# Performance work log

Hardware: AMD Instinct MI355X
Metric: run time of the kernel (lower is better)

The kernel has to match this reference:

```python
import jax, jax.numpy as jnp
import numpy as np

C = 64  # in_channels == out_channels (required by final view)

def setup_inputs() -> dict:
    key = jax.random.key(0)
    ks = jax.random.split(key, 7)
    x = jax.random.normal(ks[0], (2, C, 16, 16, 16), dtype=jnp.float32)
    s = 1.0 / np.sqrt(C)
    Wq = jax.random.uniform(ks[1], (C, C), jnp.float32, -s, s)
    bq = jax.random.uniform(ks[2], (C,), jnp.float32, -s, s)
    Wk = jax.random.uniform(ks[3], (C, C), jnp.float32, -s, s)
    bk = jax.random.uniform(ks[4], (C,), jnp.float32, -s, s)
    Wv = jax.random.uniform(ks[5], (C, C), jnp.float32, -s, s)
    bv = jax.random.uniform(ks[6], (C,), jnp.float32, -s, s)
    return {"x": x, "Wq": Wq, "bq": bq, "Wk": Wk, "bk": bk, "Wv": Wv, "bv": bv}

def _proj(x, W, b):
    # 1x1x1 Conv3d == per-voxel channel GEMM; x: [B,C,D,H,W]
    return jnp.einsum('oc,bcdhw->bodhw', W, x) + b[None, :, None, None, None]

def reference(x, Wq, bq, Wk, bk, Wv, bv):
    B, Cin, D, H, W = x.shape
    q = _proj(x, Wq, bq).reshape(B, C, -1)  # [B,C,N]
    k = _proj(x, Wk, bk).reshape(B, C, -1)
    v = _proj(x, Wv, bv).reshape(B, C, -1)
    # attention[b,i,j] = softmax_j(q_i . k_j); NOTE: unscaled, as in the source
    attn = jax.nn.softmax(jnp.einsum('bci,bcj->bij', q, k), axis=-1)
    out = jnp.einsum('bcj,bij->bci', v, attn)  # out_i = sum_j a_ij v_j
    return out.reshape(x.shape)
```

## Files before the change

### kernel.cpp

```cpp
#include <hip/hip_runtime.h>
#include <math.h>

#define CCH 64
#define NVOX 4096
#define NB 2
#define RS 72
#define TS 136

typedef _Float16 f16x8 __attribute__((ext_vector_type(8)));
typedef _Float16 f16x4 __attribute__((ext_vector_type(4)));
typedef __fp16   g16x2 __attribute__((ext_vector_type(2)));
typedef float f32x4 __attribute__((ext_vector_type(4)));

__global__ __launch_bounds__(256) void qkv_proj(
    const float* __restrict__ x,
    const float* __restrict__ Wq, const float* __restrict__ bq,
    const float* __restrict__ Wk, const float* __restrict__ bk,
    const float* __restrict__ Wv, const float* __restrict__ bv,
    _Float16* __restrict__ qh, _Float16* __restrict__ kh, _Float16* __restrict__ vh)
{
    __shared__ float Ws[3 * 64 * 64];
    __shared__ float xs[64 * 32];
    const int t  = threadIdx.x;
    const int b  = blockIdx.x >> 7;
    const int i0 = (blockIdx.x & 127) * 32;

    {
        const float4* Wq4 = (const float4*)Wq;
        const float4* Wk4 = (const float4*)Wk;
        const float4* Wv4 = (const float4*)Wv;
        float4* Ws4 = (float4*)Ws;
#pragma unroll
        for (int s = 0; s < 4; ++s) {
            int idx = t + 256 * s;
            Ws4[idx]        = Wq4[idx];
            Ws4[1024 + idx] = Wk4[idx];
            Ws4[2048 + idx] = Wv4[idx];
        }
    }
    {
        int cc = t >> 2;
        int m0 = (t & 3) * 8;
        const float* src = x + ((b * CCH + cc) * NVOX) + i0 + m0;
#pragma unroll
        for (int s = 0; s < 8; ++s) xs[cc * 32 + m0 + s] = src[s];
    }
    __syncthreads();

    const int vox = t & 31;
    const int c0  = (t >> 5) * 8;

#pragma unroll
    for (int m = 0; m < 3; ++m) {
        const float* Wm  = &Ws[m * 4096];
        const float* bia = (m == 0) ? bq : (m == 1) ? bk : bv;
        float acc[8];
#pragma unroll
        for (int j = 0; j < 8; ++j) acc[j] = bia[c0 + j];
        for (int cc = 0; cc < 64; cc += 4) {
            float xv0 = xs[(cc + 0) * 32 + vox];
            float xv1 = xs[(cc + 1) * 32 + vox];
            float xv2 = xs[(cc + 2) * 32 + vox];
            float xv3 = xs[(cc + 3) * 32 + vox];
#pragma unroll
            for (int j = 0; j < 8; ++j) {
                float4 w = *(const float4*)&Wm[(c0 + j) * 64 + cc];
                acc[j] = fmaf(w.x, xv0, acc[j]);
                acc[j] = fmaf(w.y, xv1, acc[j]);
                acc[j] = fmaf(w.z, xv2, acc[j]);
                acc[j] = fmaf(w.w, xv3, acc[j]);
            }
        }
        if (m < 2) {
            f16x8 hv;
#pragma unroll
            for (int j = 0; j < 8; ++j) hv[j] = (_Float16)acc[j];
            _Float16* dst = ((m == 0) ? qh : kh) + ((b * NVOX) + i0 + vox) * CCH + c0;
            *(f16x8*)dst = hv;
        } else {
#pragma unroll
            for (int j = 0; j < 8; ++j)
                vh[(b * CCH + c0 + j) * NVOX + i0 + vox] = (_Float16)acc[j];
        }
    }
}

template <int SPLIT>
__global__ __launch_bounds__(256) void attn(
    const _Float16* __restrict__ qh, const _Float16* __restrict__ kh,
    const _Float16* __restrict__ vh,
    _Float16* __restrict__ po,
    float* __restrict__ ml,
    float* __restrict__ out)
{
    __shared__ _Float16 ksl[2][64 * RS];
    __shared__ _Float16 vsl[2][64 * RS];

    constexpr int LS = (SPLIT == 8) ? 3 : (SPLIT == 4) ? 2 : (SPLIT == 2) ? 1 : 0;
    const int t    = threadIdx.x;
    const int h    = blockIdx.x & (SPLIT - 1);
    const int tile = blockIdx.x >> LS;
    const int b    = tile >> 5;
    const int i0   = (tile & 31) * 128;

    const int lane = t & 63;
    const int w    = t >> 6;
    const int q4   = lane >> 4;
    const int n    = lane & 15;

    const int row = t >> 2;
    const int c0  = (t & 3) * 16;
    const int JT  = 64 / SPLIT;

    auto load_tile = [&](int jt, float4 r[4]) {
        const int j0 = (h * JT + jt) * 64;
        const float4* ks = (const float4*)&kh[((size_t)(b * NVOX) + j0 + row) * CCH + c0];
        r[0] = ks[0]; r[1] = ks[1];
        const float4* vs = (const float4*)&vh[((size_t)b * CCH + row) * NVOX + j0 + c0];
        r[2] = vs[0]; r[3] = vs[1];
    };
    auto store_tile = [&](int buf, const float4 r[4]) {
        *(float4*)&ksl[buf][row * RS + c0]     = r[0];
        *(float4*)&ksl[buf][row * RS + c0 + 8] = r[1];
        *(float4*)&vsl[buf][row * RS + c0]     = r[2];
        *(float4*)&vsl[buf][row * RS + c0 + 8] = r[3];
    };

    f16x8 aq[2][2];
#pragma unroll
    for (int g = 0; g < 2; ++g) {
        const _Float16* qrow =
            qh + ((size_t)(b * NVOX) + i0 + w * 32 + g * 16 + n) * CCH + q4 * 8;
        aq[g][0] = *(const f16x8*)(qrow);
        aq[g][1] = *(const f16x8*)(qrow + 32);
    }

    float4 stg[4];
    load_tile(0, stg);
    store_tile(0, stg);

    float m_prev[2] = {-1e30f, -1e30f}, l[2] = {0.f, 0.f};
    f32x4 o[2][4];
#pragma unroll
    for (int g = 0; g < 2; ++g)
#pragma unroll
        for (int mt = 0; mt < 4; ++mt) o[g][mt] = (f32x4){0.f, 0.f, 0.f, 0.f};

    __syncthreads();

    for (int jt = 0; jt < JT; ++jt) {
        const int buf = jt & 1;
        if (jt + 1 < JT) load_tile(jt + 1, stg);

        f32x4 s[2][4];
#pragma unroll
        for (int g = 0; g < 2; ++g)
#pragma unroll
            for (int nt = 0; nt < 4; ++nt) s[g][nt] = (f32x4){0.f, 0.f, 0.f, 0.f};
#pragma unroll
        for (int ks = 0; ks < 2; ++ks) {
#pragma unroll
            for (int nt = 0; nt < 4; ++nt) {
                f16x8 ak = *(const f16x8*)&ksl[buf][(nt * 16 + n) * RS + ks * 32 + q4 * 8];
                s[0][nt] = __builtin_amdgcn_mfma_f32_16x16x32_f16(ak, aq[0][ks], s[0][nt], 0, 0, 0);
                s[1][nt] = __builtin_amdgcn_mfma_f32_16x16x32_f16(ak, aq[1][ks], s[1][nt], 0, 0, 0);
            }
        }

        f16x4 bp[2][4];
        float alpha[2];
#pragma unroll
        for (int g = 0; g < 2; ++g) {
            float mx = -1e30f;
#pragma unroll
            for (int nt = 0; nt < 4; ++nt)
#pragma unroll
                for (int r = 0; r < 4; ++r) mx = fmaxf(mx, s[g][nt][r]);
            mx = fmaxf(mx, __shfl_xor(mx, 16, 64));
            mx = fmaxf(mx, __shfl_xor(mx, 32, 64));
            const float mn = fmaxf(m_prev[g], mx);

            float p[4][4], sum = 0.f;
#pragma unroll
            for (int nt = 0; nt < 4; ++nt)
#pragma unroll
                for (int r = 0; r < 4; ++r) {
                    p[nt][r] = __expf(s[g][nt][r] - mn);
                    sum += p[nt][r];
                }
            sum += __shfl_xor(sum, 16, 64);
            sum += __shfl_xor(sum, 32, 64);

            alpha[g]  = __expf(m_prev[g] - mn);
            l[g]      = l[g] * alpha[g] + sum;
            m_prev[g] = mn;

#pragma unroll
            for (int nt = 0; nt < 4; ++nt) {
                union { g16x2 g2[2]; f16x4 h4; } u;
                u.g2[0] = __builtin_amdgcn_cvt_pkrtz(p[nt][0], p[nt][1]);
                u.g2[1] = __builtin_amdgcn_cvt_pkrtz(p[nt][2], p[nt][3]);
                bp[g][nt] = u.h4;
            }
        }

#pragma unroll
        for (int g = 0; g < 2; ++g)
#pragma unroll
            for (int mt = 0; mt < 4; ++mt)
#pragma unroll
                for (int r = 0; r < 4; ++r) o[g][mt][r] *= alpha[g];

#pragma unroll
        for (int nt = 0; nt < 4; ++nt) {
#pragma unroll
            for (int mt = 0; mt < 4; ++mt) {
                f16x4 av = *(const f16x4*)&vsl[buf][(mt * 16 + n) * RS + nt * 16 + q4 * 4];
                o[0][mt] = __builtin_amdgcn_mfma_f32_16x16x16f16(av, bp[0][nt], o[0][mt], 0, 0, 0);
                o[1][mt] = __builtin_amdgcn_mfma_f32_16x16x16f16(av, bp[1][nt], o[1][mt], 0, 0, 0);
            }
        }

        if (jt + 1 < JT) {
            __syncthreads();
            store_tile(buf ^ 1, stg);
            __syncthreads();
        }
    }

    if (SPLIT > 1) {
        __syncthreads();
        _Float16* tb = &ksl[0][0];
#pragma unroll
        for (int g = 0; g < 2; ++g)
#pragma unroll
            for (int mt = 0; mt < 4; ++mt)
#pragma unroll
                for (int r = 0; r < 4; ++r)
                    tb[(mt * 16 + q4 * 4 + r) * TS + w * 32 + g * 16 + n] =
                        (_Float16)o[g][mt][r];
#pragma unroll
        for (int g = 0; g < 2; ++g) {
            if (q4 == 0) {
                const int ig = i0 + w * 32 + g * 16 + n;
                float2* mlp = (float2*)&ml[((size_t)(b * SPLIT + h) * NVOX + ig) * 2];
                *mlp = make_float2(m_prev[g], l[g]);
            }
        }
        __syncthreads();
        const int cr = t >> 2;
        const int ib = (t & 3) * 32;
        const size_t base = ((size_t)(b * SPLIT + h) * 64 + cr) * NVOX + i0 + ib;
#pragma unroll
        for (int u = 0; u < 4; ++u) {
            f16x8 vv = *(const f16x8*)&tb[cr * TS + ib + u * 8];
            *(f16x8*)&po[base + u * 8] = vv;
        }
    } else {
#pragma unroll
        for (int g = 0; g < 2; ++g) {
            const int ig = i0 + w * 32 + g * 16 + n;
            const float inv = 1.0f / l[g];
#pragma unroll
            for (int mt = 0; mt < 4; ++mt)
#pragma unroll
                for (int r = 0; r < 4; ++r)
                    out[(size_t)(b * CCH + mt * 16 + q4 * 4 + r) * NVOX + ig] =
                        o[g][mt][r] * inv;
        }
    }
}

template <int SPLIT>
__global__ __launch_bounds__(256) void combine(
    const _Float16* __restrict__ po, const float* __restrict__ ml,
    float* __restrict__ out)
{
    __shared__ float wls[SPLIT * 64];
    const int t  = threadIdx.x;
    const int b  = blockIdx.x >> 6;
    const int i0 = (blockIdx.x & 63) * 64;

    if (t < 64) {
        const int i = i0 + t;
        float mv[SPLIT], lv[SPLIT], M = -1e30f;
#pragma unroll
        for (int h = 0; h < SPLIT; ++h) {
            mv[h] = ml[((size_t)(b * SPLIT + h) * NVOX + i) * 2 + 0];
            lv[h] = ml[((size_t)(b * SPLIT + h) * NVOX + i) * 2 + 1];
            M = fmaxf(M, mv[h]);
        }
        float den = 0.f;
#pragma unroll
        for (int h = 0; h < SPLIT; ++h) den += lv[h] * __expf(mv[h] - M);
        const float inv = 1.0f / den;
#pragma unroll
        for (int h = 0; h < SPLIT; ++h) wls[h * 64 + t] = __expf(mv[h] - M) * inv;
    }
    __syncthreads();

    const int c  = t >> 2;
    const int iq = t & 3;
    float acc[16];
#pragma unroll
    for (int u = 0; u < 16; ++u) acc[u] = 0.f;
#pragma unroll
    for (int h = 0; h < SPLIT; ++h) {
        const f16x8* src = (const f16x8*)&po[((size_t)(b * SPLIT + h) * 64 + c) * NVOX + i0 + iq * 16];
        const float* wp  = &wls[h * 64 + iq * 16];
#pragma unroll
        for (int u = 0; u < 2; ++u) {
            f16x8 f = src[u];
#pragma unroll
            for (int e = 0; e < 8; ++e)
                acc[u * 8 + e] = fmaf((float)f[e], wp[u * 8 + e], acc[u * 8 + e]);
        }
    }
    float4* dst = (float4*)&out[(size_t)(b * CCH + c) * NVOX + i0 + iq * 16];
#pragma unroll
    for (int u = 0; u < 4; ++u)
        dst[u] = make_float4(acc[u * 4], acc[u * 4 + 1], acc[u * 4 + 2], acc[u * 4 + 3]);
}

extern "C" void kernel_launch(void* const* d_in, const int* in_sizes, int n_in,
                              void* d_out, int out_size, void* d_ws, size_t ws_size,
                              hipStream_t stream)
{
    const float* x  = (const float*)d_in[0];
    const float* Wq = (const float*)d_in[1];
    const float* bq = (const float*)d_in[2];
    const float* Wk = (const float*)d_in[3];
    const float* bk = (const float*)d_in[4];
    const float* Wv = (const float*)d_in[5];
    const float* bv = (const float*)d_in[6];
    float* out = (float*)d_out;

    _Float16* qh = (_Float16*)d_ws;
    _Float16* kh = qh + NB * NVOX * CCH;
    _Float16* vh = kh + NB * NVOX * CCH;
    _Float16* po = vh + NB * NVOX * CCH;
    const size_t qkv_bytes = (size_t)3 * NB * NVOX * CCH * sizeof(_Float16);

    qkv_proj<<<NB * (NVOX / 32), 256, 0, stream>>>(x, Wq, bq, Wk, bk, Wv, bv, qh, kh, vh);

    const size_t need8 = qkv_bytes +
        (size_t)NB * 8 * 64 * NVOX * sizeof(_Float16) + (size_t)NB * 8 * NVOX * 2 * sizeof(float);
    const size_t need4 = qkv_bytes +
        (size_t)NB * 4 * 64 * NVOX * sizeof(_Float16) + (size_t)NB * 4 * NVOX * 2 * sizeof(float);
    const size_t need2 = qkv_bytes +
        (size_t)NB * 2 * 64 * NVOX * sizeof(_Float16) + (size_t)NB * 2 * NVOX * 2 * sizeof(float);

    if (ws_size >= need8) {
        float* ml = (float*)(po + (size_t)NB * 8 * 64 * NVOX);
        attn<8><<<NB * 32 * 8, 256, 0, stream>>>(qh, kh, vh, po, ml, out);
        combine<8><<<NB * 64, 256, 0, stream>>>(po, ml, out);
    } else if (ws_size >= need4) {
        float* ml = (float*)(po + (size_t)NB * 4 * 64 * NVOX);
        attn<4><<<NB * 32 * 4, 256, 0, stream>>>(qh, kh, vh, po, ml, out);
        combine<4><<<NB * 64, 256, 0, stream>>>(po, ml, out);
    } else if (ws_size >= need2) {
        float* ml = (float*)(po + (size_t)NB * 2 * 64 * NVOX);
        attn<2><<<NB * 32 * 2, 256, 0, stream>>>(qh, kh, vh, po, ml, out);
        combine<2><<<NB * 64, 256, 0, stream>>>(po, ml, out);
    } else {
        attn<1><<<NB * 32, 256, 0, stream>>>(qh, kh, vh, nullptr, nullptr, out);
    }
}
```

Measured before the change: 109.1 us.

## Load K/V tiles directly into registers, dropping LDS staging and barriers

The attention kernel stops staging K and V tiles through double-buffered shared memory. Each wave now loads its MFMA operand fragments straight from global memory into registers, with two register sets ping-ponged to prefetch the next tile, and the per-tile __syncthreads are gone. This removes LDS traffic and block-wide barriers, but each of the four waves now loads the full K/V tile redundantly from global/L2. It also needs many more registers, which may lower occupancy, and the V loads are narrow 8-byte strided reads.

```diff
diff --git a/kernel.cpp b/kernel.cpp
--- a/kernel.cpp
+++ b/kernel.cpp
@@ -4,7 +4,6 @@
 #define CCH 64
 #define NVOX 4096
 #define NB 2
-#define RS 72
 #define TS 136
 
 typedef _Float16 f16x8 __attribute__((ext_vector_type(8)));
@@ -93,8 +92,7 @@
     float* __restrict__ ml,
     float* __restrict__ out)
 {
-    __shared__ _Float16 ksl[2][64 * RS];
-    __shared__ _Float16 vsl[2][64 * RS];
+    __shared__ _Float16 tb[64 * TS];
 
     constexpr int LS = (SPLIT == 8) ? 3 : (SPLIT == 4) ? 2 : (SPLIT == 2) ? 1 : 0;
     const int t    = threadIdx.x;
@@ -108,23 +106,9 @@
     const int q4   = lane >> 4;
     const int n    = lane & 15;
 
-    const int row = t >> 2;
-    const int c0  = (t & 3) * 16;
-    const int JT  = 64 / SPLIT;
-
-    auto load_tile = [&](int jt, float4 r[4]) {
-        const int j0 = (h * JT + jt) * 64;
-        const float4* ks = (const float4*)&kh[((size_t)(b * NVOX) + j0 + row) * CCH + c0];
-        r[0] = ks[0]; r[1] = ks[1];
-        const float4* vs = (const float4*)&vh[((size_t)b * CCH + row) * NVOX + j0 + c0];
-        r[2] = vs[0]; r[3] = vs[1];
-    };
-    auto store_tile = [&](int buf, const float4 r[4]) {
-        *(float4*)&ksl[buf][row * RS + c0]     = r[0];
-        *(float4*)&ksl[buf][row * RS + c0 + 8] = r[1];
-        *(float4*)&vsl[buf][row * RS + c0]     = r[2];
-        *(float4*)&vsl[buf][row * RS + c0 + 8] = r[3];
-    };
+    const int JT = 64 / SPLIT;
+    const _Float16* kbase = kh + (size_t)b * NVOX * CCH;
+    const _Float16* vbase = vh + (size_t)b * CCH * NVOX;
 
     f16x8 aq[2][2];
 #pragma unroll
@@ -135,10 +119,6 @@
         aq[g][1] = *(const f16x8*)(qrow + 32);
     }
 
-    float4 stg[4];
-    load_tile(0, stg);
-    store_tile(0, stg);
-
     float m_prev[2] = {-1e30f, -1e30f}, l[2] = {0.f, 0.f};
     f32x4 o[2][4];
 #pragma unroll
@@ -146,26 +126,36 @@
 #pragma unroll
         for (int mt = 0; mt < 4; ++mt) o[g][mt] = (f32x4){0.f, 0.f, 0.f, 0.f};
 
-    __syncthreads();
-
-    for (int jt = 0; jt < JT; ++jt) {
-        const int buf = jt & 1;
-        if (jt + 1 < JT) load_tile(jt + 1, stg);
-
+    f16x8 ak0[2][4], ak1[2][4];
+    f16x4 av0[4][4], av1[4][4];
+
+    auto load_tile = [&](int jt, f16x8 (&ak)[2][4], f16x4 (&av)[4][4]) {
+        const int j0 = (h * JT + jt) * 64;
+#pragma unroll
+        for (int ks = 0; ks < 2; ++ks)
+#pragma unroll
+            for (int nt = 0; nt < 4; ++nt)
+                ak[ks][nt] = *(const f16x8*)&kbase[(size_t)(j0 + nt * 16 + n) * CCH + ks * 32 + q4 * 8];
+#pragma unroll
+        for (int nt = 0; nt < 4; ++nt)
+#pragma unroll
+            for (int mt = 0; mt < 4; ++mt)
+                av[nt][mt] = *(const f16x4*)&vbase[(size_t)(mt * 16 + n) * NVOX + j0 + nt * 16 + q4 * 4];
+    };
+
+    auto compute_tile = [&](const f16x8 (&ak)[2][4], const f16x4 (&av)[4][4]) {
         f32x4 s[2][4];
 #pragma unroll
         for (int g = 0; g < 2; ++g)
 #pragma unroll
             for (int nt = 0; nt < 4; ++nt) s[g][nt] = (f32x4){0.f, 0.f, 0.f, 0.f};
 #pragma unroll
-        for (int ks = 0; ks < 2; ++ks) {
+        for (int ks = 0; ks < 2; ++ks)
 #pragma unroll
             for (int nt = 0; nt < 4; ++nt) {
-                f16x8 ak = *(const f16x8*)&ksl[buf][(nt * 16 + n) * RS + ks * 32 + q4 * 8];
-                s[0][nt] = __builtin_amdgcn_mfma_f32_16x16x32_f16(ak, aq[0][ks], s[0][nt], 0, 0, 0);
-                s[1][nt] = __builtin_amdgcn_mfma_f32_16x16x32_f16(ak, aq[1][ks], s[1][nt], 0, 0, 0);
-            }
-        }
+                s[0][nt] = __builtin_amdgcn_mfma_f32_16x16x32_f16(ak[ks][nt], aq[0][ks], s[0][nt], 0, 0, 0);
+                s[1][nt] = __builtin_amdgcn_mfma_f32_16x16x32_f16(ak[ks][nt], aq[1][ks], s[1][nt], 0, 0, 0);
+            }
 
         f16x4 bp[2][4];
         float alpha[2];
@@ -212,25 +202,23 @@
                 for (int r = 0; r < 4; ++r) o[g][mt][r] *= alpha[g];
 
 #pragma unroll
-        for (int nt = 0; nt < 4; ++nt) {
+        for (int nt = 0; nt < 4; ++nt)
 #pragma unroll
             for (int mt = 0; mt < 4; ++mt) {
-                f16x4 av = *(const f16x4*)&vsl[buf][(mt * 16 + n) * RS + nt * 16 + q4 * 4];
-                o[0][mt] = __builtin_amdgcn_mfma_f32_16x16x16f16(av, bp[0][nt], o[0][mt], 0, 0, 0);
-                o[1][mt] = __builtin_amdgcn_mfma_f32_16x16x16f16(av, bp[1][nt], o[1][mt], 0, 0, 0);
-            }
-        }
-
-        if (jt + 1 < JT) {
-            __syncthreads();
-            store_tile(buf ^ 1, stg);
-            __syncthreads();
-        }
+                o[0][mt] = __builtin_amdgcn_mfma_f32_16x16x16f16(av[nt][mt], bp[0][nt], o[0][mt], 0, 0, 0);
+                o[1][mt] = __builtin_amdgcn_mfma_f32_16x16x16f16(av[nt][mt], bp[1][nt], o[1][mt], 0, 0, 0);
+            }
+    };
+
+    load_tile(0, ak0, av0);
+    for (int jt = 0; jt < JT; jt += 2) {
+        if (jt + 1 < JT) load_tile(jt + 1, ak1, av1);
+        compute_tile(ak0, av0);
+        if (jt + 2 < JT) load_tile(jt + 2, ak0, av0);
+        if (jt + 1 < JT) compute_tile(ak1, av1);
     }
 
     if (SPLIT > 1) {
-        __syncthreads();
-        _Float16* tb = &ksl[0][0];
 #pragma unroll
         for (int g = 0; g < 2; ++g)
 #pragma unroll
```

New measurement: 131.2 us. 20.3% more time.

## Swizzle K tile in LDS, defer row-sum reduction, add split-16 path

Applied to the files above, without the earlier changes.

Stores the K tile in shared memory with an XOR swizzle instead of padded rows to avoid bank conflicts on MFMA operand reads. Moves the cross-lane row-sum reduction out of the inner loop to the end, since the rescale factor is uniform across lanes. Adds an occupancy hint of 3 blocks per CU and a 16-way key split when workspace allows, trading more partial-output traffic in the combine step for more parallel blocks.

```diff
diff --git a/kernel.cpp b/kernel.cpp
--- a/kernel.cpp
+++ b/kernel.cpp
@@ -4,7 +4,7 @@
 #define CCH 64
 #define NVOX 4096
 #define NB 2
-#define RS 72
+#define VRS 72
 #define TS 136
 
 typedef _Float16 f16x8 __attribute__((ext_vector_type(8)));
@@ -86,17 +86,17 @@
 }
 
 template <int SPLIT>
-__global__ __launch_bounds__(256) void attn(
+__global__ __launch_bounds__(256, 3) void attn(
     const _Float16* __restrict__ qh, const _Float16* __restrict__ kh,
     const _Float16* __restrict__ vh,
     _Float16* __restrict__ po,
     float* __restrict__ ml,
     float* __restrict__ out)
 {
-    __shared__ _Float16 ksl[2][64 * RS];
-    __shared__ _Float16 vsl[2][64 * RS];
-
-    constexpr int LS = (SPLIT == 8) ? 3 : (SPLIT == 4) ? 2 : (SPLIT == 2) ? 1 : 0;
+    __shared__ _Float16 smem[2 * 64 * 64 + 2 * 64 * VRS];
+
+    constexpr int LS = (SPLIT == 16) ? 4 : (SPLIT == 8) ? 3 :
+                       (SPLIT == 4) ? 2 : (SPLIT == 2) ? 1 : 0;
     const int t    = threadIdx.x;
     const int h    = blockIdx.x & (SPLIT - 1);
     const int tile = blockIdx.x >> LS;
@@ -107,23 +107,28 @@
     const int w    = t >> 6;
     const int q4   = lane >> 4;
     const int n    = lane & 15;
+    const int nx   = n & 7;
+
+    auto kb = [&](int buf) -> _Float16* { return smem + buf * 4096; };
+    auto vb = [&](int buf) -> _Float16* { return smem + 8192 + buf * 64 * VRS; };
 
     const int row = t >> 2;
-    const int c0  = (t & 3) * 16;
+    const int c2  = t & 3;
     const int JT  = 64 / SPLIT;
 
     auto load_tile = [&](int jt, float4 r[4]) {
         const int j0 = (h * JT + jt) * 64;
-        const float4* ks = (const float4*)&kh[((size_t)(b * NVOX) + j0 + row) * CCH + c0];
+        const float4* ks = (const float4*)&kh[((size_t)(b * NVOX) + j0 + row) * CCH + c2 * 16];
         r[0] = ks[0]; r[1] = ks[1];
-        const float4* vs = (const float4*)&vh[((size_t)b * CCH + row) * NVOX + j0 + c0];
+        const float4* vs = (const float4*)&vh[((size_t)b * CCH + row) * NVOX + j0 + c2 * 16];
         r[2] = vs[0]; r[3] = vs[1];
     };
     auto store_tile = [&](int buf, const float4 r[4]) {
-        *(float4*)&ksl[buf][row * RS + c0]     = r[0];
-        *(float4*)&ksl[buf][row * RS + c0 + 8] = r[1];
-        *(float4*)&vsl[buf][row * RS + c0]     = r[2];
-        *(float4*)&vsl[buf][row * RS + c0 + 8] = r[3];
+        const int rx = row & 7;
+        *(float4*)&kb(buf)[row * 64 + ((2 * c2) ^ rx) * 8]     = r[0];
+        *(float4*)&kb(buf)[row * 64 + ((2 * c2 + 1) ^ rx) * 8] = r[1];
+        *(float4*)&vb(buf)[row * VRS + c2 * 16]     = r[2];
+        *(float4*)&vb(buf)[row * VRS + c2 * 16 + 8] = r[3];
     };
 
     f16x8 aq[2][2];
@@ -158,14 +163,14 @@
 #pragma unroll
             for (int nt = 0; nt < 4; ++nt) s[g][nt] = (f32x4){0.f, 0.f, 0.f, 0.f};
 #pragma unroll
-        for (int ks = 0; ks < 2; ++ks) {
+        for (int ks = 0; ks < 2; ++ks)
 #pragma unroll
             for (int nt = 0; nt < 4; ++nt) {
-                f16x8 ak = *(const f16x8*)&ksl[buf][(nt * 16 + n) * RS + ks * 32 + q4 * 8];
+                f16x8 ak = *(const f16x8*)&kb(buf)[(nt * 16 + n) * 64 +
+                                                   (((ks * 4 + q4) ^ nx) * 8)];
                 s[0][nt] = __builtin_amdgcn_mfma_f32_16x16x32_f16(ak, aq[0][ks], s[0][nt], 0, 0, 0);
                 s[1][nt] = __builtin_amdgcn_mfma_f32_16x16x32_f16(ak, aq[1][ks], s[1][nt], 0, 0, 0);
             }
-        }
 
         f16x4 bp[2][4];
         float alpha[2];
@@ -188,9 +193,6 @@
                     p[nt][r] = __expf(s[g][nt][r] - mn);
                     sum += p[nt][r];
                 }
-            sum += __shfl_xor(sum, 16, 64);
-            sum += __shfl_xor(sum, 32, 64);
-
             alpha[g]  = __expf(m_prev[g] - mn);
             l[g]      = l[g] * alpha[g] + sum;
             m_prev[g] = mn;
@@ -212,14 +214,13 @@
                 for (int r = 0; r < 4; ++r) o[g][mt][r] *= alpha[g];
 
 #pragma unroll
-        for (int nt = 0; nt < 4; ++nt) {
+        for (int nt = 0; nt < 4; ++nt)
 #pragma unroll
             for (int mt = 0; mt < 4; ++mt) {
-                f16x4 av = *(const f16x4*)&vsl[buf][(mt * 16 + n) * RS + nt * 16 + q4 * 4];
+                f16x4 av = *(const f16x4*)&vb(buf)[(mt * 16 + n) * VRS + nt * 16 + q4 * 4];
                 o[0][mt] = __builtin_amdgcn_mfma_f32_16x16x16f16(av, bp[0][nt], o[0][mt], 0, 0, 0);
                 o[1][mt] = __builtin_amdgcn_mfma_f32_16x16x16f16(av, bp[1][nt], o[1][mt], 0, 0, 0);
             }
-        }
 
         if (jt + 1 < JT) {
             __syncthreads();
@@ -228,9 +229,18 @@
         }
     }
 
+    float l_tot[2];
+#pragma unroll
+    for (int g = 0; g < 2; ++g) {
+        float lv = l[g];
+        lv += __shfl_xor(lv, 16, 64);
+        lv += __shfl_xor(lv, 32, 64);
+        l_tot[g] = lv;
+    }
+
     if (SPLIT > 1) {
         __syncthreads();
-        _Float16* tb = &ksl[0][0];
+        _Float16* tb = smem;
 #pragma unroll
         for (int g = 0; g < 2; ++g)
 #pragma unroll
@@ -244,7 +254,7 @@
             if (q4 == 0) {
                 const int ig = i0 + w * 32 + g * 16 + n;
                 float2* mlp = (float2*)&ml[((size_t)(b * SPLIT + h) * NVOX + ig) * 2];
-                *mlp = make_float2(m_prev[g], l[g]);
+                *mlp = make_float2(m_prev[g], l_tot[g]);
             }
         }
         __syncthreads();
@@ -260,7 +270,7 @@
 #pragma unroll
         for (int g = 0; g < 2; ++g) {
             const int ig = i0 + w * 32 + g * 16 + n;
-            const float inv = 1.0f / l[g];
+            const float inv = 1.0f / l_tot[g];
 #pragma unroll
             for (int mt = 0; mt < 4; ++mt)
 #pragma unroll
@@ -343,22 +353,24 @@
 
     qkv_proj<<<NB * (NVOX / 32), 256, 0, stream>>>(x, Wq, bq, Wk, bk, Wv, bv, qh, kh, vh);
 
-    const size_t need8 = qkv_bytes +
-        (size_t)NB * 8 * 64 * NVOX * sizeof(_Float16) + (size_t)NB * 8 * NVOX * 2 * sizeof(float);
-    const size_t need4 = qkv_bytes +
-        (size_t)NB * 4 * 64 * NVOX * sizeof(_Float16) + (size_t)NB * 4 * NVOX * 2 * sizeof(float);
-    const size_t need2 = qkv_bytes +
-        (size_t)NB * 2 * 64 * NVOX * sizeof(_Float16) + (size_t)NB * 2 * NVOX * 2 * sizeof(float);
-
-    if (ws_size >= need8) {
+    auto need = [&](int sp) {
+        return qkv_bytes + (size_t)NB * sp * 64 * NVOX * sizeof(_Float16)
+                         + (size_t)NB * sp * NVOX * 2 * sizeof(float);
+    };
+
+    if (ws_size >= need(16)) {
+        float* ml = (float*)(po + (size_t)NB * 16 * 64 * NVOX);
+        attn<16><<<NB * 32 * 16, 256, 0, stream>>>(qh, kh, vh, po, ml, out);
+        combine<16><<<NB * 64, 256, 0, stream>>>(po, ml, out);
+    } else if (ws_size >= need(8)) {
         float* ml = (float*)(po + (size_t)NB * 8 * 64 * NVOX);
         attn<8><<<NB * 32 * 8, 256, 0, stream>>>(qh, kh, vh, po, ml, out);
         combine<8><<<NB * 64, 256, 0, stream>>>(po, ml, out);
-    } else if (ws_size >= need4) {
+    } else if (ws_size >= need(4)) {
         float* ml = (float*)(po + (size_t)NB * 4 * 64 * NVOX);
         attn<4><<<NB * 32 * 4, 256, 0, stream>>>(qh, kh, vh, po, ml, out);
         combine<4><<<NB * 64, 256, 0, stream>>>(po, ml, out);
-    } else if (ws_size >= need2) {
+    } else if (ws_size >= need(2)) {
         float* ml = (float*)(po + (size_t)NB * 2 * 64 * NVOX);
         attn<2><<<NB * 32 * 2, 256, 0, stream>>>(qh, kh, vh, po, ml, out);
         combine<2><<<NB * 64, 256, 0, stream>>>(po, ml, out);
```

Result: slower. 117.4 us (+7.6%).
